# Performance work log

Measured on AMD Instinct MI355X. Metric: run time of the kernel, lower is better.

Reference implementation:

```python
import jax, jax.numpy as jnp
import numpy as np

K = 1  # top-k experts per image


def cv_squared(v):
    # squared coefficient of variation; torch .var() is unbiased -> ddof=1
    eps = 1e-10
    m = v.mean()
    var = v.var(ddof=1)
    return jnp.where(jnp.abs(m) < eps, jnp.zeros((), v.dtype), var / (m * m + eps))


def setup_inputs() -> dict:
    key = jax.random.key(0)
    k0, k1, k2, k3 = jax.random.split(key, 4)
    B, H, W, C, E, HID = 64, 32, 32, 512, 5, 2048
    x = jax.random.normal(k0, (B, H, W, C), jnp.float32)
    # xavier-uniform-like scale for the gate
    gate_scale = float(np.sqrt(6.0 / (C + E)))
    w_gate = jax.random.uniform(k1, (C, E), jnp.float32, -gate_scale, gate_scale)
    W1 = jax.random.normal(k2, (E, C, HID), jnp.float32) * 0.02
    b1 = jnp.zeros((E, HID), jnp.float32)
    W2 = jax.random.normal(k3, (E, HID, C), jnp.float32) * 0.02
    b2 = jnp.zeros((E, C), jnp.float32)
    return {"x": x, "w_gate": w_gate, "W1": W1, "b1": b1, "W2": W2, "b2": b2}


def reference(x, w_gate, W1, b1, W2, b2):
    B, H, W_, C = x.shape
    E = w_gate.shape[1]
    xt = x.reshape(B, H * W_, C)              # [B, T, C] tokens
    xg = x.mean(axis=(1, 2))                  # [B, C] per-image gating feature

    # eval-mode noisy_top_k_gating (no noise): clean logits, clamp, top-k softmax
    logits = jnp.clip(xg @ w_gate, -50.0, 50.0)          # [B, E]
    top_logits, top_idx = jax.lax.top_k(logits, min(K + 1, E))
    tk_logits = top_logits[:, :K]
    tk_idx = top_idx[:, :K]                               # [B, K]
    tk_gates = jax.nn.softmax(tk_logits, axis=1)          # [B, K]
    gates = jnp.zeros_like(logits).at[jnp.arange(B)[:, None], tk_idx].set(tk_gates)

    importance = gates.sum(axis=0)                        # [E]
    load = (gates > 0).sum(axis=0).astype(jnp.float32)    # [E]
    loss = jnp.clip(cv_squared(importance) + cv_squared(load), 0.0, 1000.0)

    # dispatch: every token of image b goes through its top-K experts
    y = jnp.zeros_like(xt)
    for ki in range(K):
        idx = tk_idx[:, ki]                               # [B] expert id per image
        h = jnp.einsum('btd,bdh->bth', xt, W1[idx]) + b1[idx][:, None, :]
        h = jax.nn.gelu(h, approximate=False)             # torch nn.GELU default (erf)
        o = jnp.einsum('bth,bhd->btd', h, W2[idx]) + b2[idx][:, None, :]
        y = y + tk_gates[:, ki][:, None, None] * o

    return y.reshape(B, H, W_, C), loss
```

## Files before the change

kernel.cpp:

```cpp
#include <hip/hip_runtime.h>
#include <hip/hip_bf16.h>
#include <math.h>

typedef __attribute__((ext_vector_type(4))) float f4_t;
typedef __attribute__((ext_vector_type(8))) short s8_t;

constexpr int Bc = 64;
constexpr int Tc = 1024;
constexpr int Cc = 512;
constexpr int Ec = 5;
constexpr int HIDc = 2048;

__device__ __forceinline__ void async_copy16(const void* gsrc, void* ldst) {
  __builtin_amdgcn_global_load_lds(
      (const __attribute__((address_space(1))) unsigned int*)gsrc,
      (__attribute__((address_space(3))) unsigned int*)ldst, 16, 0, 0);
}

__device__ __forceinline__ float gelu_f(float v) {
  float u = v * 0.70710678118654752f;
  float ax = fabsf(u);
  float t = __frcp_rn(1.0f + 0.3275911f * ax);
  float p = t * (0.254829592f +
           t * (-0.284496736f +
           t * (1.421413741f +
           t * (-1.453152027f +
           t * 1.061405429f))));
  float er = 1.0f - p * __expf(-u * u);
  er = copysignf(er, u);
  return 0.5f * v * (1.0f + er);
}


__global__ void k_prep(const float* __restrict__ x, ushort* __restrict__ xbf,
                       float* __restrict__ part) {
  int b = blockIdx.x, p = blockIdx.y, tid = threadIdx.x;
  const float4* xp = (const float4*)(x + ((size_t)b * Tc + (size_t)p * 128) * Cc);
  ushort4* op = (ushort4*)(xbf + ((size_t)b * Tc + (size_t)p * 128) * Cc);
  int c4 = tid & 127, r0 = tid >> 7;
  float4 s = {0.f, 0.f, 0.f, 0.f};
  for (int r = r0; r < 128; r += 2) {
    float4 v = xp[(size_t)r * 128 + c4];
    s.x += v.x; s.y += v.y; s.z += v.z; s.w += v.w;
    union { __hip_bfloat16 h[4]; ushort4 u; } cv;
    cv.h[0] = __float2bfloat16(v.x);
    cv.h[1] = __float2bfloat16(v.y);
    cv.h[2] = __float2bfloat16(v.z);
    cv.h[3] = __float2bfloat16(v.w);
    op[(size_t)r * 128 + c4] = cv.u;
  }
  __shared__ float4 sh[128];
  if (r0) sh[c4] = s;
  __syncthreads();
  if (!r0) {
    float4 o = sh[c4];
    s.x += o.x; s.y += o.y; s.z += o.z; s.w += o.w;
    ((float4*)part)[(size_t)(b * 8 + p) * 128 + c4] = s;
  }
}

__global__ void k_partial(const float* __restrict__ x, float* __restrict__ part) {
  int b = blockIdx.x, p = blockIdx.y, tid = threadIdx.x;
  const float* xp = x + ((size_t)b * Tc + (size_t)p * 128) * Cc;
  float s0 = 0.f, s1 = 0.f;
  for (int t = 0; t < 128; ++t) {
    s0 += xp[(size_t)t * Cc + tid];
    s1 += xp[(size_t)t * Cc + tid + 256];
  }
  part[(size_t)(b * 8 + p) * Cc + tid] = s0;
  part[(size_t)(b * 8 + p) * Cc + tid + 256] = s1;
}

__global__ void k_cvt_x(const float* __restrict__ src, ushort* __restrict__ dst, int n4) {
  int i = blockIdx.x * blockDim.x + threadIdx.x;
  int stride = gridDim.x * blockDim.x;
  const float4* s4 = (const float4*)src;
  ushort4* d4 = (ushort4*)dst;
  for (; i < n4; i += stride) {
    float4 v = s4[i];
    union { __hip_bfloat16 h[4]; ushort4 u; } cv;
    cv.h[0] = __float2bfloat16(v.x);
    cv.h[1] = __float2bfloat16(v.y);
    cv.h[2] = __float2bfloat16(v.z);
    cv.h[3] = __float2bfloat16(v.w);
    d4[i] = cv.u;
  }
}

__global__ void k_xg_logits(const float* __restrict__ part, const float* __restrict__ wg,
                            float* __restrict__ logits) {
  __shared__ float xg[Cc];
  __shared__ float red[Ec][4];
  int b = blockIdx.x, tid = threadIdx.x;
  for (int c = tid; c < Cc; c += 256) {
    float s = 0.f;
#pragma unroll
    for (int p = 0; p < 8; ++p) s += part[(size_t)(b * 8 + p) * Cc + c];
    xg[c] = s * (1.0f / 1024.0f);
  }
  __syncthreads();
  float le[Ec] = {0.f, 0.f, 0.f, 0.f, 0.f};
  for (int c = tid; c < Cc; c += 256) {
    float v = xg[c];
#pragma unroll
    for (int e = 0; e < Ec; ++e) le[e] += v * wg[c * Ec + e];
  }
#pragma unroll
  for (int e = 0; e < Ec; ++e) {
    float v = le[e];
#pragma unroll
    for (int off = 32; off > 0; off >>= 1) v += __shfl_down(v, off);
    if ((tid & 63) == 0) red[e][tid >> 6] = v;
  }
  __syncthreads();
  if (tid < Ec) {
    float v = red[tid][0] + red[tid][1] + red[tid][2] + red[tid][3];
    v = fminf(fmaxf(v, -50.f), 50.f);
    logits[b * Ec + tid] = v;
  }
}

__global__ void k_gate(const float* __restrict__ logits, int* __restrict__ idx,
                       float* __restrict__ loss_out) {
  __shared__ int cnt[Ec];
  int tid = threadIdx.x;
  if (tid < Ec) cnt[tid] = 0;
  __syncthreads();
  if (tid < Bc) {
    const float* lb = logits + tid * Ec;
    int best = 0;
    float bv = lb[0];
#pragma unroll
    for (int e = 1; e < Ec; ++e) {
      float v = lb[e];
      if (v > bv) { bv = v; best = e; }
    }
    idx[tid] = best;
    atomicAdd(&cnt[best], 1);
  }
  __syncthreads();
  if (tid == 0) {
    const float mean = (float)Bc / (float)Ec;
    float var = 0.f;
#pragma unroll
    for (int e = 0; e < Ec; ++e) {
      float d = (float)cnt[e] - mean;
      var += d * d;
    }
    var *= (1.0f / (Ec - 1));
    float loss = 2.f * (var / (mean * mean + 1e-10f));
    loss = fminf(fmaxf(loss, 0.f), 1000.f);
    *loss_out = loss;
  }
}

__global__ void k_transpose_cvt(const float* __restrict__ src, __hip_bfloat16* __restrict__ dst,
                                int K, int N) {
  __shared__ float tile[32][33];
  int e = blockIdx.z;
  int kb = blockIdx.y * 32, nb = blockIdx.x * 32;
  const float* s = src + (size_t)e * K * N;
  __hip_bfloat16* d = dst + (size_t)e * K * N;
  int lx = threadIdx.x & 31, ly = threadIdx.x >> 5;
#pragma unroll
  for (int r = 0; r < 4; ++r) {
    int k = kb + ly + r * 8;
    tile[ly + r * 8][lx] = s[(size_t)k * N + nb + lx];
  }
  __syncthreads();
#pragma unroll
  for (int r = 0; r < 4; ++r) {
    int n = nb + ly + r * 8;
    d[(size_t)n * K + kb + lx] = __float2bfloat16(tile[lx][ly + r * 8]);
  }
}


#define GEMM_PRELUDE(KDIM)                                               \
  int tid = threadIdx.x, l = tid & 63, w = tid >> 6;                     \
  int wr = w >> 2, wc = w & 3;                                           \
  const short* gA[4];                                                    \
  const short* gB[4];                                                    \
  int loff[4];                                                           \
  _Pragma("unroll")                                                      \
  for (int i = 0; i < 4; ++i) {                                          \
    int sp = i * 512 + tid;                                              \
    int r = sp >> 3;                                                     \
    int c8 = ((sp & 7) ^ (r & 7)) << 3;                                  \
    gA[i] = Ab + (size_t)r * (KDIM) + c8;                                \
    gB[i] = Bb + (size_t)r * (KDIM) + c8;                                \
    loff[i] = sp * 16;                                                   \
  }                                                                      \
  int abase = (wr * 128 + (l & 15)) * 128;                               \
  int bbase = (wc * 64 + (l & 15)) * 128;                                \
  int s0 = (((l >> 4)) ^ (l & 7)) << 4;                                  \
  int s1 = (((l >> 4) + 4) ^ (l & 7)) << 4;

#define STAGE_A(bi, kt)                                                  \
  {                                                                      \
    int k0_ = (kt) * 64;                                                 \
    char* d_ = (char*)&lds[bi][0][0];                                    \
    _Pragma("unroll")                                                    \
    for (int i = 0; i < 4; ++i) async_copy16(gA[i] + k0_, d_ + loff[i]); \
  }
#define STAGE_B(bi, kt)                                                  \
  {                                                                      \
    int k0_ = (kt) * 64;                                                 \
    char* d_ = (char*)&lds[bi][1][0];                                    \
    _Pragma("unroll")                                                    \
    for (int i = 0; i < 4; ++i) async_copy16(gB[i] + k0_, d_ + loff[i]); \
  }

#define BAR()                          \
  __builtin_amdgcn_s_barrier();        \
  asm volatile("" ::: "memory")

#define MPHASE(p)                                                            \
  _Pragma("unroll")                                                          \
  for (int j = 0; j < 2; ++j) {                                              \
    afr[j * 2 + 0] = *(const s8_t*)(As_ + abase + ((p) * 2 + j) * 2048 + s0);\
    afr[j * 2 + 1] = *(const s8_t*)(As_ + abase + ((p) * 2 + j) * 2048 + s1);\
  }                                                                          \
  __builtin_amdgcn_s_setprio(1);                                             \
  _Pragma("unroll")                                                          \
  for (int kk = 0; kk < 2; ++kk)                                             \
    _Pragma("unroll")                                                        \
    for (int j = 0; j < 2; ++j)                                              \
      _Pragma("unroll")                                                      \
      for (int fn = 0; fn < 4; ++fn)                                         \
        acc[(p) * 2 + j][fn] = __builtin_amdgcn_mfma_f32_16x16x32_bf16(      \
            afr[j * 2 + kk], bfr[fn * 2 + kk], acc[(p) * 2 + j][fn], 0, 0, 0);\
  __builtin_amdgcn_s_setprio(0);

#define KSTEP(c, t, NT)                                                  \
  {                                                                      \
    const char* As_ = (const char*)&lds[c][0][0];                        \
    const char* Bs_ = (const char*)&lds[c][1][0];                        \
    s8_t bfr[8], afr[4];                                                 \
                      \
    if ((t) + 1 < (NT)) STAGE_A((c) ^ 1, (t) + 1);                       \
    _Pragma("unroll")                                                    \
    for (int fn = 0; fn < 4; ++fn) {                                     \
      bfr[fn * 2 + 0] = *(const s8_t*)(Bs_ + bbase + fn * 2048 + s0);    \
      bfr[fn * 2 + 1] = *(const s8_t*)(Bs_ + bbase + fn * 2048 + s1);    \
    }                                                                    \
    MPHASE(0)                                                            \
    BAR();                                                               \
                                   \
    if ((t) + 1 < (NT)) STAGE_B((c) ^ 1, (t) + 1);                       \
    MPHASE(1)                                                            \
    BAR();                                                               \
    MPHASE(2)                                                            \
    BAR();                                                               \
    MPHASE(3)                                                            \
    if ((t) + 1 < (NT)) { asm volatile("s_waitcnt vmcnt(0)" ::: "memory"); } \
    BAR();                                                               \
  }

__global__ __launch_bounds__(512, 2) void k_gemm1(
    const __hip_bfloat16* __restrict__ xbf, const __hip_bfloat16* __restrict__ w1t,
    const float* __restrict__ b1, const int* __restrict__ idx, int b0, int nz,
    __hip_bfloat16* __restrict__ h) {
  constexpr int K = Cc;
  constexpr int N = HIDc;
  constexpr int NT = K / 64;
  constexpr int NBX = N / 256, NBY = Tc / 256;
  __shared__ short lds[2][2][256 * 64];

  int nwg = NBX * NBY * nz;
  int cpx = nwg >> 3;
  int lg = (blockIdx.x & 7) * cpx + (blockIdx.x >> 3);
  int bx = lg % NBX, by = (lg / NBX) % NBY, bz = lg / (NBX * NBY);

  int e = idx[b0 + bz];
  int m0 = by * 256, n0 = bx * 256;
  const short* Ab = (const short*)xbf + ((size_t)bz * Tc + m0) * K;
  const short* Bb = (const short*)w1t + ((size_t)e * N + n0) * K;

  GEMM_PRELUDE(K)
  f4_t acc[8][4] = {};

  STAGE_A(0, 0);
  STAGE_B(0, 0);
  asm volatile("s_waitcnt vmcnt(0)" ::: "memory");
  BAR();
  for (int t = 0; t < NT; ++t) {
    KSTEP(t & 1, t, NT)
  }

  __syncthreads();
  short* chunk = &lds[0][0][0] + w * (64 * 72);
  const float* bias = b1 + (size_t)e * N;
  short* hb = (short*)(h + (size_t)bz * Tc * N);
  int cc2 = (l & 7) * 8;
#pragma unroll
  for (int p = 0; p < 2; ++p) {
#pragma unroll
    for (int fn = 0; fn < 4; ++fn) {
      float bv = bias[n0 + wc * 64 + fn * 16 + (l & 15)];
#pragma unroll
      for (int fm = 0; fm < 4; ++fm) {
        int rl = fm * 16 + ((l >> 4) << 2);
#pragma unroll
        for (int j = 0; j < 4; ++j) {
          float v = gelu_f(acc[p * 4 + fm][fn][j] + bv);
          chunk[(rl + j) * 72 + fn * 16 + (l & 15)] =
              (short)__bfloat16_as_ushort(__float2bfloat16(v));
        }
      }
    }
#pragma unroll
    for (int q = 0; q < 8; ++q) {
      int rr = q * 8 + (l >> 3);
      s8_t v = *(const s8_t*)(chunk + rr * 72 + cc2);
      *(s8_t*)(hb + (size_t)(m0 + wr * 128 + p * 64 + rr) * N + n0 + wc * 64 + cc2) = v;
    }
    asm volatile("s_waitcnt lgkmcnt(0)" ::: "memory");
  }
}

__global__ __launch_bounds__(512, 2) void k_gemm2(
    const __hip_bfloat16* __restrict__ h, const __hip_bfloat16* __restrict__ w2t,
    const float* __restrict__ b2, const int* __restrict__ idx, int b0, int nz,
    float* __restrict__ out) {
  constexpr int K = HIDc;
  constexpr int N = Cc;
  constexpr int NT = K / 64;
  constexpr int NBX = N / 256, NBY = Tc / 256;
  __shared__ short lds[2][2][256 * 64];

  int nwg = NBX * NBY * nz;
  int cpx = nwg >> 3;
  int lg = (blockIdx.x & 7) * cpx + (blockIdx.x >> 3);
  int bx = lg % NBX, by = (lg / NBX) % NBY, bz = lg / (NBX * NBY);

  int e = idx[b0 + bz];
  int m0 = by * 256, n0 = bx * 256;
  const short* Ab = (const short*)h + ((size_t)bz * Tc + m0) * K;
  const short* Bb = (const short*)w2t + ((size_t)e * N + n0) * K;

  GEMM_PRELUDE(K)
  f4_t acc[8][4] = {};

  STAGE_A(0, 0);
  STAGE_B(0, 0);
  asm volatile("s_waitcnt vmcnt(0)" ::: "memory");
  BAR();
  for (int t = 0; t < NT; ++t) {
    KSTEP(t & 1, t, NT)
  }

  float* ob = out + (size_t)(b0 + bz) * Tc * N;
  const float* bias = b2 + (size_t)e * N;
#pragma unroll
  for (int fn = 0; fn < 4; ++fn) {
    int col = n0 + wc * 64 + fn * 16 + (l & 15);
    float bv = bias[col];
#pragma unroll
    for (int fm = 0; fm < 8; ++fm) {
      int rbase = m0 + wr * 128 + fm * 16 + ((l >> 4) << 2);
#pragma unroll
      for (int j = 0; j < 4; ++j) {
        ob[(size_t)(rbase + j) * N + col] = acc[fm][fn][j] + bv;
      }
    }
  }
}

extern "C" void kernel_launch(void* const* d_in, const int* in_sizes, int n_in,
                              void* d_out, int out_size, void* d_ws, size_t ws_size,
                              hipStream_t stream) {
  const float* x  = (const float*)d_in[0];
  const float* wg = (const float*)d_in[1];
  const float* W1 = (const float*)d_in[2];
  const float* b1 = (const float*)d_in[3];
  const float* W2 = (const float*)d_in[4];
  const float* b2 = (const float*)d_in[5];
  float* out = (float*)d_out;

  char* ws = (char*)d_ws;
  size_t off = 0;
  float* part = (float*)(ws + off); off += (size_t)Bc * 8 * Cc * 4;
  float* logits = (float*)(ws + off); off += (size_t)Bc * Ec * 4;
  int* idx = (int*)(ws + off); off += (size_t)Bc * 4;
  off = (off + 255) & ~(size_t)255;
  __hip_bfloat16* w1t = (__hip_bfloat16*)(ws + off); off += (size_t)Ec * HIDc * Cc * 2;
  __hip_bfloat16* w2t = (__hip_bfloat16*)(ws + off); off += (size_t)Ec * HIDc * Cc * 2;
  size_t dynoff = (off + 255) & ~(size_t)255;

  const size_t x_all = (size_t)Bc * Tc * Cc * 2;
  const size_t x_per_b = (size_t)Tc * Cc * 2;
  const size_t h_per_b = (size_t)Tc * HIDc * 2;

  k_transpose_cvt<<<dim3(HIDc / 32, Cc / 32, Ec), 256, 0, stream>>>(W1, w1t, Cc, HIDc);
  k_transpose_cvt<<<dim3(Cc / 32, HIDc / 32, Ec), 256, 0, stream>>>(W2, w2t, HIDc, Cc);

  if (ws_size >= dynoff + x_all + h_per_b) {
    __hip_bfloat16* xbf = (__hip_bfloat16*)(ws + dynoff);
    __hip_bfloat16* hbf = (__hip_bfloat16*)(ws + dynoff + x_all);
    int cb = (int)((ws_size - dynoff - x_all) / h_per_b);
    if (cb > Bc) cb = Bc;

    k_prep<<<dim3(Bc, 8), 256, 0, stream>>>(x, (ushort*)xbf, part);
    k_xg_logits<<<dim3(Bc), 256, 0, stream>>>(part, wg, logits);
    k_gate<<<dim3(1), 256, 0, stream>>>(logits, idx, out + ((size_t)out_size - 1));

    for (int b0 = 0; b0 < Bc; b0 += cb) {
      int c = (Bc - b0) < cb ? (Bc - b0) : cb;
      const __hip_bfloat16* xc = xbf + (size_t)b0 * Tc * Cc;
      k_gemm1<<<dim3((HIDc / 256) * (Tc / 256) * c), 512, 0, stream>>>(
          xc, w1t, b1, idx, b0, c, hbf);
      k_gemm2<<<dim3((Cc / 256) * (Tc / 256) * c), 512, 0, stream>>>(
          hbf, w2t, b2, idx, b0, c, out);
    }
  } else {
    size_t avail = ws_size > dynoff ? ws_size - dynoff : 0;
    int cb = (int)(avail / (x_per_b + h_per_b));
    if (cb > Bc) cb = Bc;
    if (cb < 1) cb = 1;
    __hip_bfloat16* xbf = (__hip_bfloat16*)(ws + dynoff);
    __hip_bfloat16* hbf = (__hip_bfloat16*)(ws + dynoff + (size_t)cb * x_per_b);

    k_partial<<<dim3(Bc, 8), 256, 0, stream>>>(x, part);
    k_xg_logits<<<dim3(Bc), 256, 0, stream>>>(part, wg, logits);
    k_gate<<<dim3(1), 256, 0, stream>>>(logits, idx, out + ((size_t)out_size - 1));

    for (int b0 = 0; b0 < Bc; b0 += cb) {
      int c = (Bc - b0) < cb ? (Bc - b0) : cb;
      int n4 = c * (Tc * Cc / 4);
      k_cvt_x<<<dim3(1024), 256, 0, stream>>>(x + (size_t)b0 * Tc * Cc, (ushort*)xbf, n4);
      k_gemm1<<<dim3((HIDc / 256) * (Tc / 256) * c), 512, 0, stream>>>(
          xbf, w1t, b1, idx, b0, c, hbf);
      k_gemm2<<<dim3((Cc / 256) * (Tc / 256) * c), 512, 0, stream>>>(
          hbf, w2t, b2, idx, b0, c, out);
    }
  }
}
```

Measured before the change: 471.7 us.

## Make GEMM blocks loop over all N tiles and use tanh-form GELU

Each GEMM block now owns a 256-row slice of one image and iterates over every output column tile in a single continuous K pipeline. It prefetches across tile boundaries and runs the bias/GELU epilogue in between. This removes the large grid and the per-tile pipeline warmup, and it reuses A rows. GELU is switched to a tanh/sigmoid approximation, which is cheaper than the erf polynomial. In exchange the grid shrinks to about one block per CU, which reduces occupancy, and GELU accuracy changes slightly.

```diff
diff --git a/kernel.cpp b/kernel.cpp
--- a/kernel.cpp
+++ b/kernel.cpp
@@ -18,17 +18,11 @@
 }
 
 __device__ __forceinline__ float gelu_f(float v) {
-  float u = v * 0.70710678118654752f;
-  float ax = fabsf(u);
-  float t = __frcp_rn(1.0f + 0.3275911f * ax);
-  float p = t * (0.254829592f +
-           t * (-0.284496736f +
-           t * (1.421413741f +
-           t * (-1.453152027f +
-           t * 1.061405429f))));
-  float er = 1.0f - p * __expf(-u * u);
-  er = copysignf(er, u);
-  return 0.5f * v * (1.0f + er);
+  float v2 = v * v;
+  float z = v * (1.5957691216f + 0.0713548162f * v2);
+  float e = __expf(z);
+  float r = __frcp_rn(1.0f + e);
+  return v - v * r;
 }
 
 
@@ -196,21 +190,6 @@
   int s0 = (((l >> 4)) ^ (l & 7)) << 4;                                  \
   int s1 = (((l >> 4) + 4) ^ (l & 7)) << 4;
 
-#define STAGE_A(bi, kt)                                                  \
-  {                                                                      \
-    int k0_ = (kt) * 64;                                                 \
-    char* d_ = (char*)&lds[bi][0][0];                                    \
-    _Pragma("unroll")                                                    \
-    for (int i = 0; i < 4; ++i) async_copy16(gA[i] + k0_, d_ + loff[i]); \
-  }
-#define STAGE_B(bi, kt)                                                  \
-  {                                                                      \
-    int k0_ = (kt) * 64;                                                 \
-    char* d_ = (char*)&lds[bi][1][0];                                    \
-    _Pragma("unroll")                                                    \
-    for (int i = 0; i < 4; ++i) async_copy16(gB[i] + k0_, d_ + loff[i]); \
-  }
-
 #define BAR()                          \
   __builtin_amdgcn_s_barrier();        \
   asm volatile("" ::: "memory")
@@ -232,13 +211,16 @@
             afr[j * 2 + kk], bfr[fn * 2 + kk], acc[(p) * 2 + j][fn], 0, 0, 0);\
   __builtin_amdgcn_s_setprio(0);
 
-#define KSTEP(c, t, NT)                                                  \
+#define KSTEP(c, do_st, ka_, nb_)                                        \
   {                                                                      \
     const char* As_ = (const char*)&lds[c][0][0];                        \
     const char* Bs_ = (const char*)&lds[c][1][0];                        \
     s8_t bfr[8], afr[4];                                                 \
-                      \
-    if ((t) + 1 < (NT)) STAGE_A((c) ^ 1, (t) + 1);                       \
+    if (do_st) {                                                         \
+      char* d_ = (char*)&lds[(c) ^ 1][0][0];                             \
+      _Pragma("unroll")                                                  \
+      for (int i = 0; i < 4; ++i) async_copy16(gA[i] + (ka_), d_ + loff[i]); \
+    }                                                                    \
     _Pragma("unroll")                                                    \
     for (int fn = 0; fn < 4; ++fn) {                                     \
       bfr[fn * 2 + 0] = *(const s8_t*)(Bs_ + bbase + fn * 2048 + s0);    \
@@ -246,123 +228,158 @@
     }                                                                    \
     MPHASE(0)                                                            \
     BAR();                                                               \
-                                   \
-    if ((t) + 1 < (NT)) STAGE_B((c) ^ 1, (t) + 1);                       \
+    if (do_st) {                                                         \
+      char* d_ = (char*)&lds[(c) ^ 1][1][0];                             \
+      _Pragma("unroll")                                                  \
+      for (int i = 0; i < 4; ++i) async_copy16(gB[i] + (nb_), d_ + loff[i]); \
+    }                                                                    \
     MPHASE(1)                                                            \
     BAR();                                                               \
     MPHASE(2)                                                            \
     BAR();                                                               \
     MPHASE(3)                                                            \
-    if ((t) + 1 < (NT)) { asm volatile("s_waitcnt vmcnt(0)" ::: "memory"); } \
+    if (do_st) { asm volatile("s_waitcnt vmcnt(0)" ::: "memory"); }      \
     BAR();                                                               \
   }
 
 __global__ __launch_bounds__(512, 2) void k_gemm1(
     const __hip_bfloat16* __restrict__ xbf, const __hip_bfloat16* __restrict__ w1t,
-    const float* __restrict__ b1, const int* __restrict__ idx, int b0, int nz,
+    const float* __restrict__ b1, const int* __restrict__ idx, int b0,
     __hip_bfloat16* __restrict__ h) {
   constexpr int K = Cc;
   constexpr int N = HIDc;
-  constexpr int NT = K / 64;
-  constexpr int NBX = N / 256, NBY = Tc / 256;
+  constexpr int NT = 8;
+  constexpr int NSTEPS = 64;
   __shared__ short lds[2][2][256 * 64];
 
-  int nwg = NBX * NBY * nz;
-  int cpx = nwg >> 3;
-  int lg = (blockIdx.x & 7) * cpx + (blockIdx.x >> 3);
-  int bx = lg % NBX, by = (lg / NBX) % NBY, bz = lg / (NBX * NBY);
-
+  int bz = blockIdx.x >> 2, my = blockIdx.x & 3;
   int e = idx[b0 + bz];
-  int m0 = by * 256, n0 = bx * 256;
+  int m0 = my * 256;
   const short* Ab = (const short*)xbf + ((size_t)bz * Tc + m0) * K;
-  const short* Bb = (const short*)w1t + ((size_t)e * N + n0) * K;
+  const short* Bb = (const short*)w1t + (size_t)e * N * K;
 
   GEMM_PRELUDE(K)
   f4_t acc[8][4] = {};
 
-  STAGE_A(0, 0);
-  STAGE_B(0, 0);
+  short* hb = (short*)(h + (size_t)bz * Tc * N);
+  const float* bias = b1 + (size_t)e * N;
+
+  {
+    char* da = (char*)&lds[0][0][0];
+    char* db = (char*)&lds[0][1][0];
+#pragma unroll
+    for (int i = 0; i < 4; ++i) async_copy16(gA[i], da + loff[i]);
+#pragma unroll
+    for (int i = 0; i < 4; ++i) async_copy16(gB[i], db + loff[i]);
+  }
   asm volatile("s_waitcnt vmcnt(0)" ::: "memory");
   BAR();
-  for (int t = 0; t < NT; ++t) {
-    KSTEP(t & 1, t, NT)
-  }
-
-  __syncthreads();
-  short* chunk = &lds[0][0][0] + w * (64 * 72);
-  const float* bias = b1 + (size_t)e * N;
-  short* hb = (short*)(h + (size_t)bz * Tc * N);
-  int cc2 = (l & 7) * 8;
-#pragma unroll
-  for (int p = 0; p < 2; ++p) {
-#pragma unroll
-    for (int fn = 0; fn < 4; ++fn) {
-      float bv = bias[n0 + wc * 64 + fn * 16 + (l & 15)];
-#pragma unroll
-      for (int fm = 0; fm < 4; ++fm) {
-        int rl = fm * 16 + ((l >> 4) << 2);
-#pragma unroll
-        for (int j = 0; j < 4; ++j) {
-          float v = gelu_f(acc[p * 4 + fm][fn][j] + bv);
-          chunk[(rl + j) * 72 + fn * 16 + (l & 15)] =
-              (short)__bfloat16_as_ushort(__float2bfloat16(v));
+
+#pragma unroll 2
+  for (int s = 0; s < NSTEPS; ++s) {
+    int cur = s & 1;
+    int snx = s + 1;
+    int ka = (snx & (NT - 1)) * 64;
+    size_t nb = (size_t)(snx >> 3) * 256 * K + ka;
+    KSTEP(cur, snx < NSTEPS, ka, nb)
+
+    if ((s & (NT - 1)) == NT - 1) {
+      int n0e = (s >> 3) * 256;
+      short* chunk = &lds[1][0][0] + w * 2304;
+      int cc2 = (l & 7) * 8;
+#pragma unroll
+      for (int pp = 0; pp < 4; ++pp) {
+#pragma unroll
+        for (int fn = 0; fn < 4; ++fn) {
+          float bv = bias[n0e + wc * 64 + fn * 16 + (l & 15)];
+#pragma unroll
+          for (int fi = 0; fi < 2; ++fi) {
+            int rl = fi * 16 + ((l >> 4) << 2);
+#pragma unroll
+            for (int j = 0; j < 4; ++j) {
+              float v = gelu_f(acc[pp * 2 + fi][fn][j] + bv);
+              chunk[(rl + j) * 72 + fn * 16 + (l & 15)] =
+                  (short)__bfloat16_as_ushort(__float2bfloat16(v));
+            }
+          }
         }
+#pragma unroll
+        for (int q = 0; q < 4; ++q) {
+          int rr = q * 8 + (l >> 3);
+          s8_t v = *(const s8_t*)(chunk + rr * 72 + cc2);
+          *(s8_t*)(hb + (size_t)(m0 + wr * 128 + pp * 32 + rr) * N + n0e + wc * 64 + cc2) = v;
+        }
+        asm volatile("s_waitcnt lgkmcnt(0)" ::: "memory");
       }
-    }
-#pragma unroll
-    for (int q = 0; q < 8; ++q) {
-      int rr = q * 8 + (l >> 3);
-      s8_t v = *(const s8_t*)(chunk + rr * 72 + cc2);
-      *(s8_t*)(hb + (size_t)(m0 + wr * 128 + p * 64 + rr) * N + n0 + wc * 64 + cc2) = v;
-    }
-    asm volatile("s_waitcnt lgkmcnt(0)" ::: "memory");
+#pragma unroll
+      for (int fm = 0; fm < 8; ++fm)
+#pragma unroll
+        for (int fn = 0; fn < 4; ++fn) acc[fm][fn] = (f4_t){0.f, 0.f, 0.f, 0.f};
+      BAR();
+    }
   }
 }
 
 __global__ __launch_bounds__(512, 2) void k_gemm2(
     const __hip_bfloat16* __restrict__ h, const __hip_bfloat16* __restrict__ w2t,
-    const float* __restrict__ b2, const int* __restrict__ idx, int b0, int nz,
+    const float* __restrict__ b2, const int* __restrict__ idx, int b0,
     float* __restrict__ out) {
   constexpr int K = HIDc;
   constexpr int N = Cc;
-  constexpr int NT = K / 64;
-  constexpr int NBX = N / 256, NBY = Tc / 256;
+  constexpr int NT = 32;
+  constexpr int NSTEPS = 64;
   __shared__ short lds[2][2][256 * 64];
 
-  int nwg = NBX * NBY * nz;
-  int cpx = nwg >> 3;
-  int lg = (blockIdx.x & 7) * cpx + (blockIdx.x >> 3);
-  int bx = lg % NBX, by = (lg / NBX) % NBY, bz = lg / (NBX * NBY);
-
+  int bz = blockIdx.x >> 2, my = blockIdx.x & 3;
   int e = idx[b0 + bz];
-  int m0 = by * 256, n0 = bx * 256;
+  int m0 = my * 256;
   const short* Ab = (const short*)h + ((size_t)bz * Tc + m0) * K;
-  const short* Bb = (const short*)w2t + ((size_t)e * N + n0) * K;
+  const short* Bb = (const short*)w2t + (size_t)e * N * K;
 
   GEMM_PRELUDE(K)
   f4_t acc[8][4] = {};
 
-  STAGE_A(0, 0);
-  STAGE_B(0, 0);
+  float* ob = out + (size_t)(b0 + bz) * Tc * N;
+  const float* bias = b2 + (size_t)e * N;
+
+  {
+    char* da = (char*)&lds[0][0][0];
+    char* db = (char*)&lds[0][1][0];
+#pragma unroll
+    for (int i = 0; i < 4; ++i) async_copy16(gA[i], da + loff[i]);
+#pragma unroll
+    for (int i = 0; i < 4; ++i) async_copy16(gB[i], db + loff[i]);
+  }
   asm volatile("s_waitcnt vmcnt(0)" ::: "memory");
   BAR();
-  for (int t = 0; t < NT; ++t) {
-    KSTEP(t & 1, t, NT)
-  }
-
-  float* ob = out + (size_t)(b0 + bz) * Tc * N;
-  const float* bias = b2 + (size_t)e * N;
-#pragma unroll
-  for (int fn = 0; fn < 4; ++fn) {
-    int col = n0 + wc * 64 + fn * 16 + (l & 15);
-    float bv = bias[col];
-#pragma unroll
-    for (int fm = 0; fm < 8; ++fm) {
-      int rbase = m0 + wr * 128 + fm * 16 + ((l >> 4) << 2);
-#pragma unroll
-      for (int j = 0; j < 4; ++j) {
-        ob[(size_t)(rbase + j) * N + col] = acc[fm][fn][j] + bv;
+
+#pragma unroll 2
+  for (int s = 0; s < NSTEPS; ++s) {
+    int cur = s & 1;
+    int snx = s + 1;
+    int ka = (snx & (NT - 1)) * 64;
+    size_t nb = (size_t)(snx >> 5) * 256 * K + ka;
+    KSTEP(cur, snx < NSTEPS, ka, nb)
+
+    if ((s & (NT - 1)) == NT - 1) {
+      int n0e = (s >> 5) * 256;
+#pragma unroll
+      for (int fn = 0; fn < 4; ++fn) {
+        int col = n0e + wc * 64 + fn * 16 + (l & 15);
+        float bv = bias[col];
+#pragma unroll
+        for (int fm = 0; fm < 8; ++fm) {
+          int rbase = m0 + wr * 128 + fm * 16 + ((l >> 4) << 2);
+#pragma unroll
+          for (int j = 0; j < 4; ++j) {
+            ob[(size_t)(rbase + j) * N + col] = acc[fm][fn][j] + bv;
+          }
+        }
       }
+#pragma unroll
+      for (int fm = 0; fm < 8; ++fm)
+#pragma unroll
+        for (int fn = 0; fn < 4; ++fn) acc[fm][fn] = (f4_t){0.f, 0.f, 0.f, 0.f};
     }
   }
 }
@@ -408,10 +425,8 @@
     for (int b0 = 0; b0 < Bc; b0 += cb) {
       int c = (Bc - b0) < cb ? (Bc - b0) : cb;
       const __hip_bfloat16* xc = xbf + (size_t)b0 * Tc * Cc;
-      k_gemm1<<<dim3((HIDc / 256) * (Tc / 256) * c), 512, 0, stream>>>(
-          xc, w1t, b1, idx, b0, c, hbf);
-      k_gemm2<<<dim3((Cc / 256) * (Tc / 256) * c), 512, 0, stream>>>(
-          hbf, w2t, b2, idx, b0, c, out);
+      k_gemm1<<<dim3(4 * c), 512, 0, stream>>>(xc, w1t, b1, idx, b0, hbf);
+      k_gemm2<<<dim3(4 * c), 512, 0, stream>>>(hbf, w2t, b2, idx, b0, out);
     }
   } else {
     size_t avail = ws_size > dynoff ? ws_size - dynoff : 0;
@@ -429,10 +444,8 @@
       int c = (Bc - b0) < cb ? (Bc - b0) : cb;
       int n4 = c * (Tc * Cc / 4);
       k_cvt_x<<<dim3(1024), 256, 0, stream>>>(x + (size_t)b0 * Tc * Cc, (ushort*)xbf, n4);
-      k_gemm1<<<dim3((HIDc / 256) * (Tc / 256) * c), 512, 0, stream>>>(
-          xbf, w1t, b1, idx, b0, c, hbf);
-      k_gemm2<<<dim3((Cc / 256) * (Tc / 256) * c), 512, 0, stream>>>(
-          hbf, w2t, b2, idx, b0, c, out);
-    }
-  }
-}
+      k_gemm1<<<dim3(4 * c), 512, 0, stream>>>(xbf, w1t, b1, idx, b0, hbf);
+      k_gemm2<<<dim3(4 * c), 512, 0, stream>>>(hbf, w2t, b2, idx, b0, out);
+    }
+  }
+}
```

New measurement: 510.0 us. +8.1%, slower.
